# Kernel tuning notes

Hardware: AMD Instinct MI355X
Metric: run time of the kernel (lower is better)

Reference implementation:

```python
import jax, jax.numpy as jnp
import numpy as np

CHW = (1, 256, 256)
NPH, NPW = 16, 16
NB = 8          # n_blocks
D = 384         # hidden_d
H = 6           # n_heads
DH = D // H     # d_head = 64
OUT = 4
PH, PW = CHW[1] // NPH, CHW[2] // NPW
IN_D = CHW[0] * PH * PW        # 256
S = NPH * NPW + 1              # 257 tokens (CLS + patches)
EPS = 1e-5                     # torch LayerNorm default


def positional_embeddings(seq_len, d):
    # matches get_positional_embeddings: sin(i/10000^(j/d)) even j, cos(i/10000^((j-1)/d)) odd j
    i = jnp.arange(seq_len, dtype=jnp.float32)[:, None]
    j = jnp.arange(d, dtype=jnp.float32)[None, :]
    j_eff = jnp.where(j % 2 == 0, j, j - 1)
    ang = i / jnp.power(jnp.float32(10000.0), j_eff / d)
    return jnp.where(j % 2 == 0, jnp.sin(ang), jnp.cos(ang))


def patchify(images):
    # (n,c,h,w) -> (n, NPH*NPW, c*PH*PW), patch flattened channel-first like patch.flatten()
    n, c, h, w = images.shape
    x = images.reshape(n, c, NPH, PH, NPW, PW)
    x = x.transpose(0, 2, 4, 1, 3, 5)  # n, nph, npw, c, ph, pw
    return x.reshape(n, NPH * NPW, c * PH * PW)


def layernorm(x, g, b):
    mu = jnp.mean(x, axis=-1, keepdims=True)
    var = jnp.mean(jnp.square(x - mu), axis=-1, keepdims=True)
    return (x - mu) * jax.lax.rsqrt(var + EPS) * g + b


def mhsa(x, Wq, bq, Wk, bk, Wv, bv):
    # x: [B,S,D]; W*: [H,DH,DH] (torch Linear convention out=x@W.T+b), b*: [H,DH]
    B = x.shape[0]
    xh = x.reshape(B, S, H, DH)
    q = jnp.einsum('bshd,hed->bshe', xh, Wq) + bq
    k = jnp.einsum('bshd,hed->bshe', xh, Wk) + bk
    v = jnp.einsum('bshd,hed->bshe', xh, Wv) + bv
    scores = jnp.einsum('bqhe,bkhe->bhqk', q, k) / jnp.float32(DH) ** 0.5
    attn = jax.nn.softmax(scores, axis=-1)
    o = jnp.einsum('bhqk,bkhe->bqhe', attn, v)
    return o.reshape(B, S, D)


def setup_inputs() -> dict:
    key = jax.random.key(0)
    ks = jax.random.split(key, 24)
    s = 0.02
    B = 64
    inp = {
        'images': jax.random.normal(ks[0], (B, *CHW), jnp.float32),
        'Wmap': jax.random.normal(ks[1], (D, IN_D), jnp.float32) * s,
        'bmap': jax.random.normal(ks[2], (D,), jnp.float32) * s,
        'cls': jax.random.uniform(ks[3], (1, D), jnp.float32),
        'ln1_g': jnp.ones((NB, D), jnp.float32),
        'ln1_b': jnp.zeros((NB, D), jnp.float32),
        'Wq': jax.random.normal(ks[4], (NB, H, DH, DH), jnp.float32) * s,
        'bq': jax.random.normal(ks[5], (NB, H, DH), jnp.float32) * s,
        'Wk': jax.random.normal(ks[6], (NB, H, DH, DH), jnp.float32) * s,
        'bk': jax.random.normal(ks[7], (NB, H, DH), jnp.float32) * s,
        'Wv': jax.random.normal(ks[8], (NB, H, DH, DH), jnp.float32) * s,
        'bv': jax.random.normal(ks[9], (NB, H, DH), jnp.float32) * s,
        'ln2_g': jnp.ones((NB, D), jnp.float32),
        'ln2_b': jnp.zeros((NB, D), jnp.float32),
        'W1': jax.random.normal(ks[10], (NB, 4 * D, D), jnp.float32) * s,
        'b1': jax.random.normal(ks[11], (NB, 4 * D), jnp.float32) * s,
        'W2': jax.random.normal(ks[12], (NB, D, 4 * D), jnp.float32) * s,
        'b2': jax.random.normal(ks[13], (NB, D), jnp.float32) * s,
        'Wout': jax.random.normal(ks[14], (OUT, D), jnp.float32) * s,
        'bout': jax.random.normal(ks[15], (OUT,), jnp.float32) * s,
    }
    return inp


def reference(images, Wmap, bmap, cls, ln1_g, ln1_b, Wq, bq, Wk, bk, Wv, bv,
              ln2_g, ln2_b, W1, b1, W2, b2, Wout, bout):
    B = images.shape[0]
    patches = patchify(images)                        # [B, S-1, IN_D]
    tokens = patches @ Wmap.T + bmap                  # [B, S-1, D]
    tokens = jnp.concatenate([jnp.broadcast_to(cls[None], (B, 1, D)), tokens], axis=1)
    out = tokens + positional_embeddings(S, D)[None]  # [B, S, D]
    for blk in range(NB):
        out = out + mhsa(layernorm(out, ln1_g[blk], ln1_b[blk]),
                         Wq[blk], bq[blk], Wk[blk], bk[blk], Wv[blk], bv[blk])
        h = layernorm(out, ln2_g[blk], ln2_b[blk])
        h = jax.nn.gelu(h @ W1[blk].T + b1[blk], approximate=False)
        out = out + (h @ W2[blk].T + b2[blk])
    cls_out = out[:, 0]                               # [B, D]
    return jax.nn.softmax(cls_out @ Wout.T + bout, axis=-1)
```

## Files before the change

### kernel.cpp

```cpp
#include <hip/hip_runtime.h>

typedef __bf16 bf16x8 __attribute__((ext_vector_type(8)));
typedef float f32x4 __attribute__((ext_vector_type(4)));
typedef unsigned short u16;
typedef unsigned short u16x4 __attribute__((ext_vector_type(4)));

typedef __attribute__((address_space(3))) unsigned int as3_u32;
typedef __attribute__((address_space(1))) unsigned int as1_u32;

static __device__ __forceinline__ float b2f(u16 u) {
    union { unsigned int ui; float f; } v; v.ui = ((unsigned int)u) << 16; return v.f;
}
static __device__ __forceinline__ u16 f2b(float f) {
    union { float f; unsigned int u; } v; v.f = f;
    unsigned int r = v.u + 0x7FFFu + ((v.u >> 16) & 1u);
    return (u16)(r >> 16);
}
static __device__ __forceinline__ float h2f(u16 u) {
    union { u16 u; _Float16 h; } v; v.u = u; return (float)v.h;
}
static __device__ __forceinline__ u16 f2h(float f) {
    union { u16 u; _Float16 h; } v; v.h = (_Float16)f; return v.u;
}
static __device__ __forceinline__ float pos_emb(int s, int d) {
    int je = d & ~1;
    float ang = (float)s * powf(10000.0f, -(float)je / 384.0f);
    return (d & 1) ? cosf(ang) : sinf(ang);
}
static __device__ __forceinline__ float gelu_f(float x) {
    float xs = x * 0.70710678118654752f;
    float ax = fabsf(xs);
    float t = __builtin_amdgcn_rcpf(1.0f + 0.3275911f * ax);
    float poly = ((((1.061405429f * t - 1.453152027f) * t + 1.421413741f) * t
                   - 0.284496736f) * t + 0.254829592f) * t;
    float e = __expf(-ax * ax);
    float erfv = 1.0f - poly * e;
    erfv = (xs < 0.f) ? -erfv : erfv;
    return 0.5f * x * (1.0f + erfv);
}
static __device__ __forceinline__ void async16(const void* g, void* l) {
    __builtin_amdgcn_global_load_lds((const as1_u32*)g, (as3_u32*)l, 16, 0, 0);
}

#define MFMA16 __builtin_amdgcn_mfma_f32_16x16x32_bf16

static __device__ __forceinline__ bf16x8 ln8(const u16* __restrict__ p, float mu, float rs,
                                             f32x4 g0, f32x4 g1, f32x4 b0, f32x4 b1) {
    u16x4 xlo = *(const u16x4*)p;
    u16x4 xhi = *(const u16x4*)(p + 4);
    u16 o[8];
#pragma unroll
    for (int j = 0; j < 4; j++) o[j]     = f2b((h2f(xlo[j]) - mu) * rs * g0[j] + b0[j]);
#pragma unroll
    for (int j = 0; j < 4; j++) o[4 + j] = f2b((h2f(xhi[j]) - mu) * rs * g1[j] + b1[j]);
    return *(bf16x8*)o;
}

template<int K>
static __device__ __forceinline__ void stage_tile(const u16* __restrict__ gbase,
                                                  u16* lds, int kt, int t) {
#pragma unroll
    for (int j = 0; j < 4; j++) {
        int o = j * 4096 + t * 16;
        int row = o >> 7;
        int c = (o >> 4) & 7;
        int gc = c ^ (row & 7);
        const u16* src = gbase + (size_t)row * K + kt * 64 + gc * 8;
        async16(src, (char*)lds + o);
    }
}

template<int K, int EPI>
__global__ __launch_bounds__(256) void k_gemm128(const u16* __restrict__ A,
                                                 const u16* __restrict__ Bw,
                                                 const float* __restrict__ bias,
                                                 u16* __restrict__ out16,
                                                 u16* __restrict__ xres) {
    __shared__ u16 lds[2][128 * 64];
    const int t = threadIdx.x;
    const int NY = gridDim.y;
    int nwg = gridDim.x * NY;
    int flat = blockIdx.x + gridDim.x * blockIdx.y;
    int q8 = nwg >> 3, r8 = nwg & 7, xcd = flat & 7, idx = flat >> 3;
    int wg = (xcd < r8 ? xcd * (q8 + 1) : r8 * (q8 + 1) + (xcd - r8) * q8) + idx;
    const int mt = wg / NY, nt = wg - mt * NY;

    const u16* Ab = A + (size_t)mt * 128 * K;
    const u16* Bb = Bw + (size_t)nt * 128 * K;
    constexpr int NKT = K / 64;
    const int lane = t & 63, w = t >> 6;
    const int wm = (w >> 1) * 64, wn = (w & 1) * 64;
    const int r = lane & 15, g = lane >> 4;

    f32x4 acc[4][4] = {};
    for (int kt = 0; kt < NKT; kt++) {
        stage_tile<K>(Ab, lds[0], kt, t);
        stage_tile<K>(Bb, lds[1], kt, t);
        asm volatile("s_waitcnt vmcnt(0)" ::: "memory");
        __builtin_amdgcn_sched_barrier(0);
        __builtin_amdgcn_s_barrier();
        __builtin_amdgcn_sched_barrier(0);
#pragma unroll
        for (int ks = 0; ks < 2; ks++) {
            bf16x8 a[4], b[4];
#pragma unroll
            for (int i = 0; i < 4; i++) {
                int ra = wm + i * 16 + r;
                int ca = (ks * 4 + g) ^ (ra & 7);
                a[i] = *(const bf16x8*)((const char*)lds[0] + ra * 128 + ca * 16);
                int rb = wn + i * 16 + r;
                int cb = (ks * 4 + g) ^ (rb & 7);
                b[i] = *(const bf16x8*)((const char*)lds[1] + rb * 128 + cb * 16);
            }
            __builtin_amdgcn_s_setprio(1);
#pragma unroll
            for (int i = 0; i < 4; i++)
#pragma unroll
                for (int jj = 0; jj < 4; jj++)
                    acc[i][jj] = MFMA16(a[i], b[jj], acc[i][jj], 0, 0, 0);
            __builtin_amdgcn_s_setprio(0);
        }
        __builtin_amdgcn_s_barrier();
    }
#pragma unroll
    for (int i = 0; i < 4; i++) {
#pragma unroll
        for (int q = 0; q < 4; q++) {
            int ml = mt * 128 + wm + i * 16 + g * 4 + q;
#pragma unroll
            for (int jj = 0; jj < 4; jj++) {
                int n = nt * 128 + wn + jj * 16 + r;
                float v = acc[i][jj][q] + bias[n];
                if (EPI == 0) {
                    out16[(size_t)ml * 1536 + n] = f2b(gelu_f(v));
                } else if (EPI == 1) {
                    if (ml < 16448) {
                        size_t o = (size_t)ml * 384 + n;
                        xres[o] = f2h(h2f(xres[o]) + v);
                    }
                } else {
                    if (ml < 64) {
                        size_t o = ((size_t)ml * 257) * 384 + n;
                        xres[o] = f2h(h2f(xres[o]) + v);
                    }
                }
            }
        }
    }
}

__global__ __launch_bounds__(64) void k_fattn(const u16* __restrict__ qb,
                                              const u16* __restrict__ kb,
                                              const u16* __restrict__ vT,
                                              u16* __restrict__ ao, int clsmode) {
    __shared__ u16 pl[32][40];
    const int lane = threadIdx.x;
    int flat = blockIdx.x;
    int bh, q0;
    if (clsmode) {
        bh = flat; q0 = 0;
    } else {
        int xcd = flat & 7, idx = flat >> 3;
        int lbh = idx / 9;
        bh = xcd * 48 + lbh;
        q0 = (idx - lbh * 9) * 32;
    }
    const int b = bh / 6, h = bh - b * 6;
    const int r = lane & 15, g = lane >> 4;

    const u16* qbase = qb + ((size_t)b * 257) * 384 + h * 64;
    const u16* kbase = kb + ((size_t)b * 257) * 384 + h * 64;
    const u16* vbase = vT + ((size_t)bh * 64) * 288;

    bf16x8 qf[2][2];
#pragma unroll
    for (int ti = 0; ti < 2; ti++)
#pragma unroll
        for (int kh = 0; kh < 2; kh++)
            qf[ti][kh] = *(const bf16x8*)(qbase + (size_t)(q0 + ti * 16 + r) * 384 + kh * 32 + g * 8);

    f32x4 accO[2][2][2] = {};
    f32x4 sum_[2] = {};

    for (int kv0 = 0; kv0 < 288; kv0 += 32) {
        bf16x8 kf[2][2];
#pragma unroll
        for (int tj = 0; tj < 2; tj++)
#pragma unroll
            for (int kh = 0; kh < 2; kh++)
                kf[tj][kh] = *(const bf16x8*)(kbase + (size_t)(kv0 + tj * 16 + r) * 384 + kh * 32 + g * 8);
        bf16x8 vf[2][2];
#pragma unroll
        for (int eT = 0; eT < 2; eT++)
#pragma unroll
            for (int tjE = 0; tjE < 2; tjE++)
                vf[eT][tjE] = *(const bf16x8*)(vbase + (size_t)(eT * 32 + tjE * 16 + r) * 288 + kv0 + g * 8);

        f32x4 s_[2][2] = {};
#pragma unroll
        for (int ti = 0; ti < 2; ti++)
#pragma unroll
            for (int tj = 0; tj < 2; tj++) {
                s_[ti][tj] = MFMA16(qf[ti][0], kf[tj][0], s_[ti][tj], 0, 0, 0);
                s_[ti][tj] = MFMA16(qf[ti][1], kf[tj][1], s_[ti][tj], 0, 0, 0);
            }
#pragma unroll
        for (int ti = 0; ti < 2; ti++) {
#pragma unroll
            for (int tj = 0; tj < 2; tj++) {
                bool bad = (kv0 + tj * 16 + r) >= 257;
#pragma unroll
                for (int q = 0; q < 4; q++) {
                    float p = bad ? 0.f : __expf(s_[ti][tj][q] * 0.125f);
                    s_[ti][tj][q] = p;
                }
                sum_[ti] += s_[ti][tj];
#pragma unroll
                for (int q = 0; q < 4; q++)
                    pl[ti * 16 + g * 4 + q][tj * 16 + r] = f2b(s_[ti][tj][q]);
            }
        }
        bf16x8 pa[2];
#pragma unroll
        for (int ti2 = 0; ti2 < 2; ti2++)
            pa[ti2] = *(const bf16x8*)&pl[ti2 * 16 + r][g * 8];
#pragma unroll
        for (int eT = 0; eT < 2; eT++)
#pragma unroll
            for (int ti2 = 0; ti2 < 2; ti2++)
#pragma unroll
                for (int tjE = 0; tjE < 2; tjE++)
                    accO[eT][ti2][tjE] = MFMA16(pa[ti2], vf[eT][tjE], accO[eT][ti2][tjE], 0, 0, 0);
    }
#pragma unroll
    for (int o = 1; o < 16; o <<= 1)
#pragma unroll
        for (int ti = 0; ti < 2; ti++)
#pragma unroll
            for (int q = 0; q < 4; q++)
                sum_[ti][q] += __shfl_xor(sum_[ti][q], o, 64);
#pragma unroll
    for (int ti = 0; ti < 2; ti++)
#pragma unroll
        for (int q = 0; q < 4; q++) {
            int qi = q0 + ti * 16 + g * 4 + q;
            if (qi < 257) {
                float inv = 1.0f / sum_[ti][q];
                u16* pao = ao + ((size_t)b * 257 + qi) * 384 + h * 64;
#pragma unroll
                for (int eT = 0; eT < 2; eT++)
#pragma unroll
                    for (int tjE = 0; tjE < 2; tjE++)
                        pao[eT * 32 + tjE * 16 + r] = f2b(accO[eT][ti][tjE][q] * inv);
            }
        }
}

__global__ __launch_bounds__(256) void k_cvt16(const void* __restrict__ src, u16* __restrict__ dst,
                                               int n, const unsigned* __restrict__ probe) {
    const bool isf32 = (*probe == 0x3F800000u);
    int i0 = (blockIdx.x * 256 + threadIdx.x) * 4;
    if (isf32) {
        const float* s = (const float*)src;
#pragma unroll
        for (int j = 0; j < 4; j++) { int i = i0 + j; if (i < n) dst[i] = f2b(s[i]); }
    } else {
        const u16* s = (const u16*)src;
#pragma unroll
        for (int j = 0; j < 4; j++) { int i = i0 + j; if (i < n) dst[i] = s[i]; }
    }
}
__global__ __launch_bounds__(256) void k_cvt32(const void* __restrict__ src, float* __restrict__ dst,
                                               int n, const unsigned* __restrict__ probe) {
    const bool isf32 = (*probe == 0x3F800000u);
    int i0 = (blockIdx.x * 256 + threadIdx.x) * 4;
    if (isf32) {
        const float* s = (const float*)src;
#pragma unroll
        for (int j = 0; j < 4; j++) { int i = i0 + j; if (i < n) dst[i] = s[i]; }
    } else {
        const u16* s = (const u16*)src;
#pragma unroll
        for (int j = 0; j < 4; j++) { int i = i0 + j; if (i < n) dst[i] = b2f(s[i]); }
    }
}

__global__ __launch_bounds__(256) void k_vtpad(u16* __restrict__ vT) {
    int idx = blockIdx.x * 256 + threadIdx.x;
    const int total = 384 * 64 * 31;
    if (idx < total) {
        int be = idx / 31; int s = 257 + (idx - be * 31);
        vT[(size_t)be * 288 + s] = 0;
    }
}

__global__ __launch_bounds__(256) void k_patch(const u16* __restrict__ img,
                                               const u16* __restrict__ Wmap,
                                               const float* __restrict__ bmap,
                                               u16* __restrict__ x) {
    const int lane = threadIdx.x & 63;
    const int wv = threadIdx.x >> 6;
    const int mt = blockIdx.x * 4 + wv;
    const int nt = blockIdx.y;
    const int m0 = mt * 32, n0 = nt * 32;
    const int r = lane & 15, kr = (lane >> 4) << 3;
    f32x4 acc[2][2] = {};
    int ma = m0 + r;
    size_t base0 = (size_t)(ma >> 8) * 65536 + (size_t)((ma >> 4) & 15) * 4096 + (size_t)(ma & 15) * 16;
    ma += 16;
    size_t base1 = (size_t)(ma >> 8) * 65536 + (size_t)((ma >> 4) & 15) * 4096 + (size_t)(ma & 15) * 16;
    const u16* pb0 = Wmap + (size_t)(n0 + r) * 256 + kr;
    const u16* pb1 = pb0 + 16 * 256;
    for (int k0 = 0; k0 < 256; k0 += 32) {
        int k = k0 + kr;
        size_t off = (size_t)(k >> 4) * 256 + (k & 15);
        bf16x8 a0 = *(const bf16x8*)(img + base0 + off);
        bf16x8 a1 = *(const bf16x8*)(img + base1 + off);
        bf16x8 b0 = *(const bf16x8*)(pb0 + k0);
        bf16x8 b1 = *(const bf16x8*)(pb1 + k0);
        acc[0][0] = MFMA16(a0, b0, acc[0][0], 0, 0, 0);
        acc[0][1] = MFMA16(a0, b1, acc[0][1], 0, 0, 0);
        acc[1][0] = MFMA16(a1, b0, acc[1][0], 0, 0, 0);
        acc[1][1] = MFMA16(a1, b1, acc[1][1], 0, 0, 0);
    }
#pragma unroll
    for (int ti = 0; ti < 2; ti++)
#pragma unroll
        for (int i = 0; i < 4; i++) {
            int m = m0 + ti * 16 + ((lane >> 4) << 2) + i;
            int b = m >> 8, p = m & 255, s = p + 1;
            u16* px = x + ((size_t)b * 257 + s) * 384;
#pragma unroll
            for (int tj = 0; tj < 2; tj++) {
                int n = n0 + tj * 16 + (lane & 15);
                px[n] = f2h(acc[ti][tj][i] + bmap[n] + pos_emb(s, n));
            }
        }
}

__global__ __launch_bounds__(384) void k_cls(const float* __restrict__ cls, u16* __restrict__ x) {
    int b = blockIdx.x, d = threadIdx.x;
    x[(size_t)b * 257 * 384 + d] = f2h(cls[d] + pos_emb(0, d));
}

__global__ __launch_bounds__(256) void k_stats(const u16* __restrict__ x,
                                               float* __restrict__ st) {
    const int lane = threadIdx.x & 63, wv = threadIdx.x >> 6;
    const int row = blockIdx.x * 16 + wv * 4 + (lane >> 4);
    const int r = lane & 15;
    const u16* px = x + (size_t)row * 384;
    f32x4 v[6]; float s = 0.f;
#pragma unroll
    for (int i = 0; i < 6; i++) {
        u16x4 x4 = *(const u16x4*)(px + i * 64 + r * 4);
#pragma unroll
        for (int j = 0; j < 4; j++) v[i][j] = h2f(x4[j]);
        s += v[i][0] + v[i][1] + v[i][2] + v[i][3];
    }
#pragma unroll
    for (int o = 1; o < 16; o <<= 1) s += __shfl_xor(s, o, 64);
    float mu = s * (1.0f / 384.0f);
    float q = 0.f;
#pragma unroll
    for (int i = 0; i < 6; i++)
#pragma unroll
        for (int j = 0; j < 4; j++) { float d = v[i][j] - mu; q += d * d; }
#pragma unroll
    for (int o = 1; o < 16; o <<= 1) q += __shfl_xor(q, o, 64);
    float rstd = rsqrtf(q * (1.0f / 384.0f) + 1e-5f);
    if (r == 0) { st[row * 2] = mu; st[row * 2 + 1] = rstd; }
}

__global__ __launch_bounds__(256) void k_ln2r(u16* __restrict__ x,
                                              const u16* __restrict__ ao,
                                              const float* __restrict__ g,
                                              const float* __restrict__ bb,
                                              u16* __restrict__ xn) {
    const int lane = threadIdx.x & 63, wv = threadIdx.x >> 6;
    const int row = blockIdx.x * 16 + wv * 4 + (lane >> 4);
    const int r = lane & 15;
    u16* px = x + (size_t)row * 384;
    const u16* pa = ao + (size_t)row * 384;
    f32x4 v[6]; float s = 0.f;
#pragma unroll
    for (int i = 0; i < 6; i++) {
        u16x4 x4 = *(const u16x4*)(px + i * 64 + r * 4);
        u16x4 a4 = *(const u16x4*)(pa + i * 64 + r * 4);
#pragma unroll
        for (int j = 0; j < 4; j++) v[i][j] = h2f(x4[j]) + b2f(a4[j]);
        s += v[i][0] + v[i][1] + v[i][2] + v[i][3];
    }
#pragma unroll
    for (int o = 1; o < 16; o <<= 1) s += __shfl_xor(s, o, 64);
    float mu = s * (1.0f / 384.0f);
    float q = 0.f;
#pragma unroll
    for (int i = 0; i < 6; i++)
#pragma unroll
        for (int j = 0; j < 4; j++) { float d = v[i][j] - mu; q += d * d; }
#pragma unroll
    for (int o = 1; o < 16; o <<= 1) q += __shfl_xor(q, o, 64);
    float rstd = rsqrtf(q * (1.0f / 384.0f) + 1e-5f);
    u16* po = xn + (size_t)row * 384;
#pragma unroll
    for (int i = 0; i < 6; i++) {
        int d0 = i * 64 + r * 4;
        u16x4 h4;
#pragma unroll
        for (int j = 0; j < 4; j++) h4[j] = f2h(v[i][j]);
        *(u16x4*)(px + d0) = h4;
        f32x4 gg = *(const f32x4*)(g + d0);
        f32x4 bv = *(const f32x4*)(bb + d0);
        u16x4 o4;
#pragma unroll
        for (int j = 0; j < 4; j++) o4[j] = f2b((v[i][j] - mu) * rstd * gg[j] + bv[j]);
        *(u16x4*)(po + d0) = o4;
    }
}

__global__ __launch_bounds__(256) void k_ln2r_cls(u16* __restrict__ x,
                                                  const u16* __restrict__ ao,
                                                  const float* __restrict__ g,
                                                  const float* __restrict__ bb,
                                                  u16* __restrict__ xnc) {
    const int lane = threadIdx.x & 63, wv = threadIdx.x >> 6;
    const int bi = blockIdx.x * 16 + wv * 4 + (lane >> 4);
    const int r = lane & 15;
    const size_t row = (size_t)bi * 257;
    u16* px = x + row * 384;
    const u16* pa = ao + row * 384;
    f32x4 v[6]; float s = 0.f;
#pragma unroll
    for (int i = 0; i < 6; i++) {
        u16x4 x4 = *(const u16x4*)(px + i * 64 + r * 4);
        u16x4 a4 = *(const u16x4*)(pa + i * 64 + r * 4);
#pragma unroll
        for (int j = 0; j < 4; j++) v[i][j] = h2f(x4[j]) + b2f(a4[j]);
        s += v[i][0] + v[i][1] + v[i][2] + v[i][3];
    }
#pragma unroll
    for (int o = 1; o < 16; o <<= 1) s += __shfl_xor(s, o, 64);
    float mu = s * (1.0f / 384.0f);
    float q = 0.f;
#pragma unroll
    for (int i = 0; i < 6; i++)
#pragma unroll
        for (int j = 0; j < 4; j++) { float d = v[i][j] - mu; q += d * d; }
#pragma unroll
    for (int o = 1; o < 16; o <<= 1) q += __shfl_xor(q, o, 64);
    float rstd = rsqrtf(q * (1.0f / 384.0f) + 1e-5f);
    u16* po = xnc + (size_t)bi * 384;
#pragma unroll
    for (int i = 0; i < 6; i++) {
        int d0 = i * 64 + r * 4;
        u16x4 h4;
#pragma unroll
        for (int j = 0; j < 4; j++) h4[j] = f2h(v[i][j]);
        *(u16x4*)(px + d0) = h4;
        f32x4 gg = *(const f32x4*)(g + d0);
        f32x4 bv = *(const f32x4*)(bb + d0);
        u16x4 o4;
#pragma unroll
        for (int j = 0; j < 4; j++) o4[j] = f2b((v[i][j] - mu) * rstd * gg[j] + bv[j]);
        *(u16x4*)(po + d0) = o4;
    }
}

__global__ __launch_bounds__(256) void k_qkv3(const u16* __restrict__ x,
                                              const float* __restrict__ st,
                                              const float* __restrict__ lg,
                                              const float* __restrict__ lb,
                                              const u16* __restrict__ Wq,
                                              const u16* __restrict__ Wk,
                                              const u16* __restrict__ Wv,
                                              const float* __restrict__ bq,
                                              const float* __restrict__ bk,
                                              const float* __restrict__ bv,
                                              u16* __restrict__ qo,
                                              u16* __restrict__ ko,
                                              u16* __restrict__ vT) {
    const int lane = threadIdx.x & 63, wv = threadIdx.x >> 6;
    int nwg = 129 * 12;
    int flat = blockIdx.x + 129 * blockIdx.y;
    int q8 = nwg >> 3, r8 = nwg & 7, xcd = flat & 7, idx = flat >> 3;
    int wg = (xcd < r8 ? xcd * (q8 + 1) : r8 * (q8 + 1) + (xcd - r8) * q8) + idx;
    int bxx = wg / 12, rest = wg - bxx * 12;

    const int mt = bxx * 4 + wv; if (mt >= 514) return;
    const int nt = rest & 1, h = rest >> 1;
    const int r = lane & 15, kr = (lane >> 4) << 3;

    const int row0 = mt * 32 + r, row1 = row0 + 16;
    const u16* xr0 = x + (size_t)row0 * 384 + h * 64;
    const u16* xr1 = x + (size_t)row1 * 384 + h * 64;
    const float mu0 = st[row0 * 2], rs0 = st[row0 * 2 + 1];
    const float mu1 = st[row1 * 2], rs1 = st[row1 * 2 + 1];
    f32x4 gA = *(const f32x4*)(lg + h * 64 + kr);
    f32x4 gB = *(const f32x4*)(lg + h * 64 + kr + 4);
    f32x4 gC = *(const f32x4*)(lg + h * 64 + 32 + kr);
    f32x4 gD = *(const f32x4*)(lg + h * 64 + 32 + kr + 4);
    f32x4 bA = *(const f32x4*)(lb + h * 64 + kr);
    f32x4 bB = *(const f32x4*)(lb + h * 64 + kr + 4);
    f32x4 bC = *(const f32x4*)(lb + h * 64 + 32 + kr);
    f32x4 bD = *(const f32x4*)(lb + h * 64 + 32 + kr + 4);

    bf16x8 a00 = ln8(xr0 + kr, mu0, rs0, gA, gB, bA, bB);
    bf16x8 a10 = ln8(xr1 + kr, mu1, rs1, gA, gB, bA, bB);
    bf16x8 a01 = ln8(xr0 + 32 + kr, mu0, rs0, gC, gD, bC, bD);
    bf16x8 a11 = ln8(xr1 + 32 + kr, mu1, rs1, gC, gD, bC, bD);

    const u16* Ws[3] = { Wq, Wk, Wv };
    const float* bs[3] = { bq, bk, bv };
#pragma unroll
    for (int ty = 0; ty < 3; ty++) {
        const u16* Bb = Ws[ty] + ((size_t)h * 64 + nt * 32) * 64;
        bf16x8 b00 = *(const bf16x8*)(Bb + (size_t)r * 64 + kr);
        bf16x8 b10 = *(const bf16x8*)(Bb + (size_t)(16 + r) * 64 + kr);
        bf16x8 b01 = *(const bf16x8*)(Bb + (size_t)r * 64 + 32 + kr);
        bf16x8 b11 = *(const bf16x8*)(Bb + (size_t)(16 + r) * 64 + 32 + kr);
        f32x4 acc[2][2] = {};
        acc[0][0] = MFMA16(a00, b00, acc[0][0], 0, 0, 0);
        acc[0][1] = MFMA16(a00, b10, acc[0][1], 0, 0, 0);
        acc[1][0] = MFMA16(a10, b00, acc[1][0], 0, 0, 0);
        acc[1][1] = MFMA16(a10, b10, acc[1][1], 0, 0, 0);
        acc[0][0] = MFMA16(a01, b01, acc[0][0], 0, 0, 0);
        acc[0][1] = MFMA16(a01, b11, acc[0][1], 0, 0, 0);
        acc[1][0] = MFMA16(a11, b01, acc[1][0], 0, 0, 0);
        acc[1][1] = MFMA16(a11, b11, acc[1][1], 0, 0, 0);
        const float* bias = bs[ty];
#pragma unroll
        for (int ti = 0; ti < 2; ti++)
#pragma unroll
            for (int i = 0; i < 4; i++) {
                int m = mt * 32 + ti * 16 + ((lane >> 4) << 2) + i;
#pragma unroll
                for (int tj = 0; tj < 2; tj++) {
                    int nl = nt * 32 + tj * 16 + (lane & 15);
                    float v = acc[ti][tj][i] + bias[h * 64 + nl];
                    if (ty == 0) {
                        qo[(size_t)m * 384 + h * 64 + nl] = f2b(v);
                    } else if (ty == 1) {
                        ko[(size_t)m * 384 + h * 64 + nl] = f2b(v);
                    } else {
                        int b = m / 257, s = m - b * 257;
                        vT[(((size_t)b * 6 + h) * 64 + nl) * 288 + s] = f2b(v);
                    }
                }
            }
    }
}

__global__ __launch_bounds__(256) void k_head(const u16* __restrict__ x,
                                              const float* __restrict__ Wout,
                                              const float* __restrict__ bout,
                                              float* __restrict__ out) {
    int t = threadIdx.x; int b = t >> 2, o = t & 3;
    const u16* px = x + (size_t)b * 257 * 384;
    const float* pw = Wout + o * 384;
    float s = 0.f;
    for (int d = 0; d < 384; d++) s += h2f(px[d]) * pw[d];
    s += bout[o];
    float mx = fmaxf(s, __shfl_xor(s, 1, 4));
    mx = fmaxf(mx, __shfl_xor(mx, 2, 4));
    float e = expf(s - mx);
    float sm = e + __shfl_xor(e, 1, 4);
    sm += __shfl_xor(sm, 2, 4);
    out[t] = e / sm;
}

extern "C" void kernel_launch(void* const* d_in, const int* in_sizes, int n_in,
                              void* d_out, int out_size, void* d_ws, size_t ws_size,
                              hipStream_t stream) {
    const unsigned* probe = (const unsigned*)d_in[4];

    char* w = (char*)d_ws;
    size_t used = 0;
    auto alloc = [&](size_t bytes) -> char* {
        char* p = w + used; used += (bytes + 255) & ~(size_t)255; return p;
    };
    u16*   x   = (u16*)  alloc(16448ull * 384 * 2);
    u16*   xn  = (u16*)  alloc(16512ull * 384 * 2);
    u16*   xnc = (u16*)  alloc(128ull * 384 * 2);
    u16*   qb  = (u16*)  alloc(16448ull * 384 * 2);
    u16*   kb  = (u16*)  alloc(16448ull * 384 * 2);
    u16*   vT  = (u16*)  alloc(384ull * 64 * 288 * 2);
    u16*   ao  = (u16*)  alloc(16448ull * 384 * 2);
    float* stx = (float*)alloc(16448ull * 2 * 4);
    u16*   imB = (u16*)  alloc(4194304ull * 2);
    u16*   WmB = (u16*)  alloc(98304ull * 2);
    u16*   WqB = (u16*)  alloc(196608ull * 2);
    u16*   WkB = (u16*)  alloc(196608ull * 2);
    u16*   WvB = (u16*)  alloc(196608ull * 2);
    u16*   W1B = (u16*)  alloc(4718592ull * 2);
    u16*   W2B = (u16*)  alloc(4718592ull * 2);
    float* prm = (float*)alloc(39172ull * 4);
    u16*   hb  = (u16*)  alloc(16512ull * 1536 * 2);
    (void)ws_size;

    float* bmapF = prm + 0;
    float* clsF  = prm + 384;
    float* ln1gF = prm + 768;
    float* ln1bF = prm + 3840;
    float* bqF   = prm + 6912;
    float* bkF   = prm + 9984;
    float* bvF   = prm + 13056;
    float* ln2gF = prm + 16128;
    float* ln2bF = prm + 19200;
    float* b1F   = prm + 22272;
    float* b2F   = prm + 34560;
    float* WoutF = prm + 37632;
    float* boutF = prm + 39168;

    dim3 B256(256);
    auto cvt16 = [&](const void* src, u16* dst, int n) {
        hipLaunchKernelGGL(k_cvt16, dim3((n + 1023) / 1024), B256, 0, stream, src, dst, n, probe);
    };
    auto cvt32 = [&](const void* src, float* dst, int n) {
        hipLaunchKernelGGL(k_cvt32, dim3((n + 1023) / 1024), B256, 0, stream, src, dst, n, probe);
    };
    cvt16(d_in[0],  imB, 4194304);
    cvt16(d_in[1],  WmB, 98304);
    cvt16(d_in[6],  WqB, 196608);
    cvt16(d_in[8],  WkB, 196608);
    cvt16(d_in[10], WvB, 196608);
    cvt16(d_in[14], W1B, 4718592);
    cvt16(d_in[16], W2B, 4718592);
    cvt32(d_in[2],  bmapF, 384);
    cvt32(d_in[3],  clsF,  384);
    cvt32(d_in[4],  ln1gF, 3072);
    cvt32(d_in[5],  ln1bF, 3072);
    cvt32(d_in[7],  bqF,   3072);
    cvt32(d_in[9],  bkF,   3072);
    cvt32(d_in[11], bvF,   3072);
    cvt32(d_in[12], ln2gF, 3072);
    cvt32(d_in[13], ln2bF, 3072);
    cvt32(d_in[15], b1F,   12288);
    cvt32(d_in[17], b2F,   3072);
    cvt32(d_in[18], WoutF, 1536);
    cvt32(d_in[19], boutF, 4);
    (void)in_sizes; (void)n_in; (void)out_size;

    hipMemsetAsync(xn + 16448ull * 384, 0, 64ull * 384 * 2, stream);
    hipMemsetAsync(xnc + 64ull * 384, 0, 64ull * 384 * 2, stream);

    hipLaunchKernelGGL(k_vtpad, dim3((384 * 64 * 31 + 255) / 256), B256, 0, stream, vT);
    hipLaunchKernelGGL(k_patch, dim3(128, 12), B256, 0, stream, imB, WmB, bmapF, x);
    hipLaunchKernelGGL(k_cls, dim3(64), dim3(384), 0, stream, clsF, x);
    for (int blk = 0; blk < 8; blk++) {
        hipLaunchKernelGGL(k_stats, dim3(1028), B256, 0, stream, x, stx);
        hipLaunchKernelGGL(k_qkv3, dim3(129, 12), B256, 0, stream, x, stx,
                           ln1gF + blk * 384, ln1bF + blk * 384,
                           WqB + (size_t)blk * 24576, WkB + (size_t)blk * 24576, WvB + (size_t)blk * 24576,
                           bqF + blk * 384, bkF + blk * 384, bvF + blk * 384,
                           qb, kb, vT);
        if (blk < 7) {
            hipLaunchKernelGGL(k_fattn, dim3(3456), dim3(64), 0, stream, qb, kb, vT, ao, 0);
            hipLaunchKernelGGL(k_ln2r, dim3(1028), B256, 0, stream, x, ao,
                               ln2gF + blk * 384, ln2bF + blk * 384, xn);
            k_gemm128<384, 0><<<dim3(129, 12), B256, 0, stream>>>(
                xn, W1B + (size_t)blk * 1536 * 384, b1F + blk * 1536, hb, nullptr);
            k_gemm128<1536, 1><<<dim3(129, 3), B256, 0, stream>>>(
                hb, W2B + (size_t)blk * 384 * 1536, b2F + blk * 384, nullptr, x);
        } else {
            hipLaunchKernelGGL(k_fattn, dim3(384), dim3(64), 0, stream, qb, kb, vT, ao, 1);
            hipLaunchKernelGGL(k_ln2r_cls, dim3(4), B256, 0, stream, x, ao,
                               ln2gF + blk * 384, ln2bF + blk * 384, xnc);
            k_gemm128<384, 0><<<dim3(1, 12), B256, 0, stream>>>(
                xnc, W1B + (size_t)blk * 1536 * 384, b1F + blk * 1536, hb, nullptr);
            k_gemm128<1536, 2><<<dim3(1, 3), B256, 0, stream>>>(
                hb, W2B + (size_t)blk * 384 * 1536, b2F + blk * 384, nullptr, x);
        }
    }
    hipLaunchKernelGGL(k_head, dim3(1), B256, 0, stream, x, WoutF, boutF, (float*)d_out);
}
```

Baseline: 1.282 ms.

## Fuse LN1 stats into W2 epilogue, convert images in patch kernel, skip unused Q

The W2 GEMM epilogue now accumulates per-row sum and sum-of-squares of the updated residual with atomics into a ping-pong stats buffer, so the separate stats kernel runs only once before the first block. The QKV kernel derives mean and rstd from these sums. The patch kernel reads the raw image and converts it to bf16 inline, which removes the separate image conversion pass. In the last block, Q projection is skipped for tiles with no CLS row. The one-pass variance formula and float atomics add some numerical risk and nondeterminism, plus a memset per block.

```diff
diff --git a/kernel.cpp b/kernel.cpp
--- a/kernel.cpp
+++ b/kernel.cpp
@@ -75,7 +75,8 @@
                                                  const u16* __restrict__ Bw,
                                                  const float* __restrict__ bias,
                                                  u16* __restrict__ out16,
-                                                 u16* __restrict__ xres) {
+                                                 u16* __restrict__ xres,
+                                                 float* __restrict__ stn) {
     __shared__ u16 lds[2][128 * 64];
     const int t = threadIdx.x;
     const int NY = gridDim.y;
@@ -127,6 +128,7 @@
 #pragma unroll
         for (int q = 0; q < 4; q++) {
             int ml = mt * 128 + wm + i * 16 + g * 4 + q;
+            float rsum = 0.f, rsq = 0.f;
 #pragma unroll
             for (int jj = 0; jj < 4; jj++) {
                 int n = nt * 128 + wn + jj * 16 + r;
@@ -136,13 +138,27 @@
                 } else if (EPI == 1) {
                     if (ml < 16448) {
                         size_t o = (size_t)ml * 384 + n;
-                        xres[o] = f2h(h2f(xres[o]) + v);
+                        u16 hv = f2h(h2f(xres[o]) + v);
+                        xres[o] = hv;
+                        float nv = h2f(hv);
+                        rsum += nv; rsq += nv * nv;
                     }
                 } else {
                     if (ml < 64) {
                         size_t o = ((size_t)ml * 257) * 384 + n;
                         xres[o] = f2h(h2f(xres[o]) + v);
                     }
+                }
+            }
+            if (EPI == 1 && ml < 16448) {
+#pragma unroll
+                for (int o = 1; o < 16; o <<= 1) {
+                    rsum += __shfl_xor(rsum, o, 64);
+                    rsq  += __shfl_xor(rsq, o, 64);
+                }
+                if (r == 0) {
+                    atomicAdd(&stn[ml * 2], rsum);
+                    atomicAdd(&stn[ml * 2 + 1], rsq);
                 }
             }
         }
@@ -294,10 +310,12 @@
     }
 }
 
-__global__ __launch_bounds__(256) void k_patch(const u16* __restrict__ img,
+__global__ __launch_bounds__(256) void k_patch(const void* __restrict__ imgraw,
                                                const u16* __restrict__ Wmap,
                                                const float* __restrict__ bmap,
-                                               u16* __restrict__ x) {
+                                               u16* __restrict__ x,
+                                               const unsigned* __restrict__ probe) {
+    const bool isf32 = (*probe == 0x3F800000u);
     const int lane = threadIdx.x & 63;
     const int wv = threadIdx.x >> 6;
     const int mt = blockIdx.x * 4 + wv;
@@ -311,11 +329,27 @@
     size_t base1 = (size_t)(ma >> 8) * 65536 + (size_t)((ma >> 4) & 15) * 4096 + (size_t)(ma & 15) * 16;
     const u16* pb0 = Wmap + (size_t)(n0 + r) * 256 + kr;
     const u16* pb1 = pb0 + 16 * 256;
+    const float* imf = (const float*)imgraw;
+    const u16* imu = (const u16*)imgraw;
     for (int k0 = 0; k0 < 256; k0 += 32) {
         int k = k0 + kr;
         size_t off = (size_t)(k >> 4) * 256 + (k & 15);
-        bf16x8 a0 = *(const bf16x8*)(img + base0 + off);
-        bf16x8 a1 = *(const bf16x8*)(img + base1 + off);
+        bf16x8 a0, a1;
+        if (isf32) {
+            u16 t0[8], t1[8];
+            f32x4 v00 = *(const f32x4*)(imf + base0 + off);
+            f32x4 v01 = *(const f32x4*)(imf + base0 + off + 4);
+            f32x4 v10 = *(const f32x4*)(imf + base1 + off);
+            f32x4 v11 = *(const f32x4*)(imf + base1 + off + 4);
+#pragma unroll
+            for (int j = 0; j < 4; j++) { t0[j] = f2b(v00[j]); t0[4 + j] = f2b(v01[j]); }
+#pragma unroll
+            for (int j = 0; j < 4; j++) { t1[j] = f2b(v10[j]); t1[4 + j] = f2b(v11[j]); }
+            a0 = *(bf16x8*)t0; a1 = *(bf16x8*)t1;
+        } else {
+            a0 = *(const bf16x8*)(imu + base0 + off);
+            a1 = *(const bf16x8*)(imu + base1 + off);
+        }
         bf16x8 b0 = *(const bf16x8*)(pb0 + k0);
         bf16x8 b1 = *(const bf16x8*)(pb1 + k0);
         acc[0][0] = MFMA16(a0, b0, acc[0][0], 0, 0, 0);
@@ -349,26 +383,16 @@
     const int row = blockIdx.x * 16 + wv * 4 + (lane >> 4);
     const int r = lane & 15;
     const u16* px = x + (size_t)row * 384;
-    f32x4 v[6]; float s = 0.f;
+    float s = 0.f, q = 0.f;
 #pragma unroll
     for (int i = 0; i < 6; i++) {
         u16x4 x4 = *(const u16x4*)(px + i * 64 + r * 4);
 #pragma unroll
-        for (int j = 0; j < 4; j++) v[i][j] = h2f(x4[j]);
-        s += v[i][0] + v[i][1] + v[i][2] + v[i][3];
-    }
-#pragma unroll
-    for (int o = 1; o < 16; o <<= 1) s += __shfl_xor(s, o, 64);
-    float mu = s * (1.0f / 384.0f);
-    float q = 0.f;
-#pragma unroll
-    for (int i = 0; i < 6; i++)
-#pragma unroll
-        for (int j = 0; j < 4; j++) { float d = v[i][j] - mu; q += d * d; }
-#pragma unroll
-    for (int o = 1; o < 16; o <<= 1) q += __shfl_xor(q, o, 64);
-    float rstd = rsqrtf(q * (1.0f / 384.0f) + 1e-5f);
-    if (r == 0) { st[row * 2] = mu; st[row * 2 + 1] = rstd; }
+        for (int j = 0; j < 4; j++) { float v = h2f(x4[j]); s += v; q += v * v; }
+    }
+#pragma unroll
+    for (int o = 1; o < 16; o <<= 1) { s += __shfl_xor(s, o, 64); q += __shfl_xor(q, o, 64); }
+    if (r == 0) { st[row * 2] = s; st[row * 2 + 1] = q; }
 }
 
 __global__ __launch_bounds__(256) void k_ln2r(u16* __restrict__ x,
@@ -478,23 +502,34 @@
                                               const float* __restrict__ bv,
                                               u16* __restrict__ qo,
                                               u16* __restrict__ ko,
-                                              u16* __restrict__ vT) {
+                                              u16* __restrict__ vT, int qskip) {
     const int lane = threadIdx.x & 63, wv = threadIdx.x >> 6;
     int nwg = 129 * 12;
     int flat = blockIdx.x + 129 * blockIdx.y;
-    int q8 = nwg >> 3, r8 = nwg & 7, xcd = flat & 7, idx = flat >> 3;
-    int wg = (xcd < r8 ? xcd * (q8 + 1) : r8 * (q8 + 1) + (xcd - r8) * q8) + idx;
+    int q8w = nwg >> 3, r8 = nwg & 7, xcd = flat & 7, idx = flat >> 3;
+    int wg = (xcd < r8 ? xcd * (q8w + 1) : r8 * (q8w + 1) + (xcd - r8) * q8w) + idx;
     int bxx = wg / 12, rest = wg - bxx * 12;
 
     const int mt = bxx * 4 + wv; if (mt >= 514) return;
     const int nt = rest & 1, h = rest >> 1;
     const int r = lane & 15, kr = (lane >> 4) << 3;
 
+    bool needq = true;
+    if (qskip) {
+        int m0 = mt * 32;
+        int rem = m0 % 257;
+        needq = (rem < 32) || (rem + 32 > 257);
+    }
+
     const int row0 = mt * 32 + r, row1 = row0 + 16;
     const u16* xr0 = x + (size_t)row0 * 384 + h * 64;
     const u16* xr1 = x + (size_t)row1 * 384 + h * 64;
-    const float mu0 = st[row0 * 2], rs0 = st[row0 * 2 + 1];
-    const float mu1 = st[row1 * 2], rs1 = st[row1 * 2 + 1];
+    float s0 = st[row0 * 2], q0s = st[row0 * 2 + 1];
+    float s1 = st[row1 * 2], q1s = st[row1 * 2 + 1];
+    float mu0 = s0 * (1.0f / 384.0f);
+    float rs0 = rsqrtf(fmaxf(q0s * (1.0f / 384.0f) - mu0 * mu0, 0.f) + 1e-5f);
+    float mu1 = s1 * (1.0f / 384.0f);
+    float rs1 = rsqrtf(fmaxf(q1s * (1.0f / 384.0f) - mu1 * mu1, 0.f) + 1e-5f);
     f32x4 gA = *(const f32x4*)(lg + h * 64 + kr);
     f32x4 gB = *(const f32x4*)(lg + h * 64 + kr + 4);
     f32x4 gC = *(const f32x4*)(lg + h * 64 + 32 + kr);
@@ -513,6 +548,7 @@
     const float* bs[3] = { bq, bk, bv };
 #pragma unroll
     for (int ty = 0; ty < 3; ty++) {
+        if (ty == 0 && !needq) continue;
         const u16* Bb = Ws[ty] + ((size_t)h * 64 + nt * 32) * 64;
         bf16x8 b00 = *(const bf16x8*)(Bb + (size_t)r * 64 + kr);
         bf16x8 b10 = *(const bf16x8*)(Bb + (size_t)(16 + r) * 64 + kr);
@@ -558,7 +594,11 @@
     const u16* px = x + (size_t)b * 257 * 384;
     const float* pw = Wout + o * 384;
     float s = 0.f;
-    for (int d = 0; d < 384; d++) s += h2f(px[d]) * pw[d];
+    for (int d = 0; d < 96; d++) {
+        u16x4 x4 = *(const u16x4*)(px + d * 4);
+#pragma unroll
+        for (int j = 0; j < 4; j++) s += h2f(x4[j]) * pw[d * 4 + j];
+    }
     s += bout[o];
     float mx = fmaxf(s, __shfl_xor(s, 1, 4));
     mx = fmaxf(mx, __shfl_xor(mx, 2, 4));
@@ -585,8 +625,8 @@
     u16*   kb  = (u16*)  alloc(16448ull * 384 * 2);
     u16*   vT  = (u16*)  alloc(384ull * 64 * 288 * 2);
     u16*   ao  = (u16*)  alloc(16448ull * 384 * 2);
-    float* stx = (float*)alloc(16448ull * 2 * 4);
-    u16*   imB = (u16*)  alloc(4194304ull * 2);
+    float* stA = (float*)alloc(16448ull * 2 * 4);
+    float* stB = (float*)alloc(16448ull * 2 * 4);
     u16*   WmB = (u16*)  alloc(98304ull * 2);
     u16*   WqB = (u16*)  alloc(196608ull * 2);
     u16*   WkB = (u16*)  alloc(196608ull * 2);
@@ -618,7 +658,6 @@
     auto cvt32 = [&](const void* src, float* dst, int n) {
         hipLaunchKernelGGL(k_cvt32, dim3((n + 1023) / 1024), B256, 0, stream, src, dst, n, probe);
     };
-    cvt16(d_in[0],  imB, 4194304);
     cvt16(d_in[1],  WmB, 98304);
     cvt16(d_in[6],  WqB, 196608);
     cvt16(d_in[8],  WkB, 196608);
@@ -644,31 +683,36 @@
     hipMemsetAsync(xnc + 64ull * 384, 0, 64ull * 384 * 2, stream);
 
     hipLaunchKernelGGL(k_vtpad, dim3((384 * 64 * 31 + 255) / 256), B256, 0, stream, vT);
-    hipLaunchKernelGGL(k_patch, dim3(128, 12), B256, 0, stream, imB, WmB, bmapF, x);
+    hipLaunchKernelGGL(k_patch, dim3(128, 12), B256, 0, stream, d_in[0], WmB, bmapF, x, probe);
     hipLaunchKernelGGL(k_cls, dim3(64), dim3(384), 0, stream, clsF, x);
+    hipLaunchKernelGGL(k_stats, dim3(1028), B256, 0, stream, x, stA);
+
+    float* stCur = stA;
+    float* stNxt = stB;
     for (int blk = 0; blk < 8; blk++) {
-        hipLaunchKernelGGL(k_stats, dim3(1028), B256, 0, stream, x, stx);
-        hipLaunchKernelGGL(k_qkv3, dim3(129, 12), B256, 0, stream, x, stx,
+        hipLaunchKernelGGL(k_qkv3, dim3(129, 12), B256, 0, stream, x, stCur,
                            ln1gF + blk * 384, ln1bF + blk * 384,
                            WqB + (size_t)blk * 24576, WkB + (size_t)blk * 24576, WvB + (size_t)blk * 24576,
                            bqF + blk * 384, bkF + blk * 384, bvF + blk * 384,
-                           qb, kb, vT);
+                           qb, kb, vT, blk == 7 ? 1 : 0);
         if (blk < 7) {
             hipLaunchKernelGGL(k_fattn, dim3(3456), dim3(64), 0, stream, qb, kb, vT, ao, 0);
             hipLaunchKernelGGL(k_ln2r, dim3(1028), B256, 0, stream, x, ao,
                                ln2gF + blk * 384, ln2bF + blk * 384, xn);
             k_gemm128<384, 0><<<dim3(129, 12), B256, 0, stream>>>(
-                xn, W1B + (size_t)blk * 1536 * 384, b1F + blk * 1536, hb, nullptr);
+                xn, W1B + (size_t)blk * 1536 * 384, b1F + blk * 1536, hb, nullptr, nullptr);
+            hipMemsetAsync(stNxt, 0, 16448ull * 2 * 4, stream);
             k_gemm128<1536, 1><<<dim3(129, 3), B256, 0, stream>>>(
-                hb, W2B + (size_t)blk * 384 * 1536, b2F + blk * 384, nullptr, x);
+                hb, W2B + (size_t)blk * 384 * 1536, b2F + blk * 384, nullptr, x, stNxt);
+            float* tmp = stCur; stCur = stNxt; stNxt = tmp;
         } else {
             hipLaunchKernelGGL(k_fattn, dim3(384), dim3(64), 0, stream, qb, kb, vT, ao, 1);
             hipLaunchKernelGGL(k_ln2r_cls, dim3(4), B256, 0, stream, x, ao,
                                ln2gF + blk * 384, ln2bF + blk * 384, xnc);
             k_gemm128<384, 0><<<dim3(1, 12), B256, 0, stream>>>(
-                xnc, W1B + (size_t)blk * 1536 * 384, b1F + blk * 1536, hb, nullptr);
+                xnc, W1B + (size_t)blk * 1536 * 384, b1F + blk * 1536, hb, nullptr, nullptr);
             k_gemm128<1536, 2><<<dim3(1, 3), B256, 0, stream>>>(
-                hb, W2B + (size_t)blk * 384 * 1536, b2F + blk * 384, nullptr, x);
+                hb, W2B + (size_t)blk * 384 * 1536, b2F + blk * 384, nullptr, x, nullptr);
         }
     }
     hipLaunchKernelGGL(k_head, dim3(1), B256, 0, stream, x, WoutF, boutF, (float*)d_out);
```

Measured after the change: 1.297 ms. About the same (+1.2%).
